# Kernel optimization log

Measured on AMD Instinct MI355X. Metric: run time of the kernel, lower is better.

Reference implementation:

```python
import jax, jax.numpy as jnp
import numpy as np

D_MODEL = 1024
NUM_HEADS = 16
PERIOD_LEN = 4096
HEAD_DIM = D_MODEL // NUM_HEADS


def setup_inputs() -> dict:
    key = jax.random.key(0)
    ks = jax.random.split(key, 10)
    B, S, D = 2, 2048, D_MODEL
    scale = 1.0 / np.sqrt(D)
    inp = {
        "x": jax.random.normal(ks[0], (B, S, D), dtype=jnp.float32),
        "wq": jax.random.normal(ks[1], (D, D), dtype=jnp.float32) * scale,
        "bq": jnp.zeros((D,), dtype=jnp.float32),
        "wk": jax.random.normal(ks[2], (D, D), dtype=jnp.float32) * scale,
        "bk": jnp.zeros((D,), dtype=jnp.float32),
        "wv": jax.random.normal(ks[3], (D, D), dtype=jnp.float32) * scale,
        "bv": jnp.zeros((D,), dtype=jnp.float32),
        "wo": jax.random.normal(ks[4], (D, D), dtype=jnp.float32) * scale,
        "bo": jnp.zeros((D,), dtype=jnp.float32),
        # original init is zeros; use small randn so bias path is non-trivial
        "rel_bias": jax.random.normal(ks[5], (PERIOD_LEN, NUM_HEADS), dtype=jnp.float32) * 0.02,
    }
    return inp


def reference(x, wq, bq, wk, bk, wv, bv, wo, bo, rel_bias):
    B, S, D = x.shape
    H, Hd = NUM_HEADS, HEAD_DIM
    q = (x @ wq + bq).reshape(B, S, H, Hd).transpose(0, 2, 1, 3)  # [B,H,S,Hd]
    k = (x @ wk + bk).reshape(B, S, H, Hd).transpose(0, 2, 1, 3)
    v = (x @ wv + bv).reshape(B, S, H, Hd).transpose(0, 2, 1, 3)
    scores = jnp.einsum('bhqd,bhkd->bhqk', q, k) / jnp.sqrt(jnp.float32(Hd))
    if S <= PERIOD_LEN:
        pos = jnp.arange(S)
        circ = (pos[:, None] - pos[None, :]) % PERIOD_LEN  # [S,S]
        bias = rel_bias[circ]                               # [S,S,H]
        scores = scores + bias.transpose(2, 0, 1)[None]     # [1,H,S,S]
    attn = jax.nn.softmax(scores, axis=-1)
    out = jnp.einsum('bhqk,bhkd->bhqd', attn, v)
    out = out.transpose(0, 2, 1, 3).reshape(B, S, D)
    return out @ wo + bo
```

## Files before the change

kernel.cpp:

```cpp
#include <hip/hip_runtime.h>
#include <hip/hip_bf16.h>

#define D_MODEL 1024
#define NHEADS  16
#define HEADD   64
#define SEQ     2048
#define PERIOD  4096
#define LOG2E   1.44269504088896340736f

typedef __attribute__((ext_vector_type(4)))  float f32x4;
typedef __attribute__((ext_vector_type(16))) float f32x16;
typedef __attribute__((ext_vector_type(4)))  float fvec4;
typedef __attribute__((ext_vector_type(8)))  short s16x8;
typedef __attribute__((ext_vector_type(4)))  short s16x4;
typedef __attribute__((ext_vector_type(2)))  int   i32x2;
typedef __attribute__((ext_vector_type(4)))  int   i32x4;

__device__ __forceinline__ short bf16_bits(float f) {
    union { float f; unsigned u; } v; v.f = f;
    unsigned r = v.u + 0x7FFFu + ((v.u >> 16) & 1u);
    return (short)(r >> 16);
}

__device__ __forceinline__ int cvt_pk_bf16(float a, float b) {
    int r;
    asm("v_cvt_pk_bf16_f32 %0, %1, %2" : "=v"(r) : "v"(a), "v"(b));
    return r;
}

__device__ __forceinline__ float exp2_hw(float x) {
    float r;
    asm("v_exp_f32 %0, %1" : "=v"(r) : "v"(x));
    return r;
}

__device__ __forceinline__ void gload_lds16(const void* g, void* l) {
    __builtin_amdgcn_global_load_lds(
        (const __attribute__((address_space(1))) void*)g,
        (__attribute__((address_space(3))) void*)l, 16, 0, 0);
}

__global__ void cvt_x(const float* __restrict__ x, short* __restrict__ xb) {
    int i = blockIdx.x * blockDim.x + threadIdx.x;
    fvec4 v = ((const fvec4*)x)[i];
    s16x4 o;
    o.x = bf16_bits(v.x); o.y = bf16_bits(v.y);
    o.z = bf16_bits(v.z); o.w = bf16_bits(v.w);
    ((s16x4*)xb)[i] = o;
}

__global__ void transpose_w4(const float* __restrict__ wq, const float* __restrict__ wk,
                             const float* __restrict__ wv, const float* __restrict__ wo,
                             short* __restrict__ wqkv, short* __restrict__ wot) {
    __shared__ float tile[64][65];
    int wsel = blockIdx.y;
    const float* src = wsel == 0 ? wq : (wsel == 1 ? wk : (wsel == 2 ? wv : wo));
    short* dst = wsel < 3 ? wqkv + wsel * 1024 * 1024 : wot;
    int bx = blockIdx.x & 15, by = blockIdx.x >> 4;
    int n0 = bx * 64, k0 = by * 64;
    int t = threadIdx.x;
    int cr = t >> 4;
    int cc = (t & 15) * 4;
    for (int i = 0; i < 4; ++i) {
        int row = cr + i * 16;
        fvec4 v = *(const fvec4*)&src[(k0 + row) * D_MODEL + n0 + cc];
        tile[row][cc+0] = v.x; tile[row][cc+1] = v.y;
        tile[row][cc+2] = v.z; tile[row][cc+3] = v.w;
    }
    __syncthreads();
    for (int i = 0; i < 4; ++i) {
        int row = cr + i * 16;
        s16x4 o;
        o.x = bf16_bits(tile[cc+0][row]);
        o.y = bf16_bits(tile[cc+1][row]);
        o.z = bf16_bits(tile[cc+2][row]);
        o.w = bf16_bits(tile[cc+3][row]);
        *(s16x4*)&dst[(n0 + row) * D_MODEL + k0 + cc] = o;
    }
}

__global__ void transpose_v(const short* __restrict__ vb, short* __restrict__ vt) {
    __shared__ short tile[64][80];
    int bh = blockIdx.y, st = blockIdx.x;
    int b = bh >> 4, h = bh & 15;
    int s0 = st * 64;
    int t = threadIdx.x;
    int row = t >> 3, ch = t & 7;
    for (int i = 0; i < 2; ++i) {
        int r = row + i * 32;
        *(s16x8*)&tile[r][ch * 8] =
            *(const s16x8*)&vb[(b * SEQ + s0 + r) * D_MODEL + h * HEADD + ch * 8];
    }
    __syncthreads();
    for (int i = 0; i < 2; ++i) {
        int d = row + i * 32;
        s16x8 o;
        #pragma unroll
        for (int j = 0; j < 8; ++j) o[j] = tile[ch * 8 + j][d];
        *(s16x8*)&vt[(b * D_MODEL + h * HEADD + d) * SEQ + s0 + ch * 8] = o;
    }
}

__global__ void build_biasq(const float* __restrict__ rb, f32x4* __restrict__ bq4) {
    int id = blockIdx.x * 256 + threadIdx.x;
    int h = id >> 12, a = id & 4095;
    f32x4 v;
    #pragma unroll
    for (int j = 0; j < 4; ++j)
        v[j] = rb[((a + j) & (PERIOD - 1)) * NHEADS + h] * LOG2E - 16.0f;
    bq4[id] = v;
}

__global__ __launch_bounds__(256, 3) void gemm_qkv(
    const short* __restrict__ A, const short* __restrict__ Bt,
    const float* __restrict__ biasq, const float* __restrict__ biask,
    const float* __restrict__ biasv,
    short* __restrict__ qb, short* __restrict__ kb, short* __restrict__ vb)
{
    __shared__ short As[2][128 * 64];
    __shared__ short Bs[2][64 * 64];
    int tid = threadIdx.x;
    int lane = tid & 63, wid = tid >> 6;
    int ln = lane & 15, g = lane >> 4;
    int wr = (wid >> 1) * 64, wc = (wid & 1) * 32;

    int bid = blockIdx.x;
    int xcd = bid & 7, slot = bid >> 3;
    int mb = xcd * 4 + (slot / 48);
    int nb = slot % 48;
    int m0 = mb * 128, n0 = nb * 64;

    int wsel = n0 >> 10;
    const float* bias = wsel == 0 ? biasq : (wsel == 1 ? biask : biasv);
    short* dst = wsel == 0 ? qb : (wsel == 1 ? kb : vb);
    float osc = wsel == 0 ? (0.125f * LOG2E) : 1.0f;
    int ncol0 = n0 & 1023;

    f32x4 acc[4][2] = {};

    auto STAGE = [&](int kt, int bi) {
        #pragma unroll
        for (int i = 0; i < 4; ++i) {
            int idx = i * 256 + tid;
            int row = idx >> 3, ch = idx & 7;
            int gch = ch ^ (row & 7);
            gload_lds16(&A[(m0 + row) * 1024 + kt + gch * 8],
                        (char*)&As[bi][0] + (i * 256 + wid * 64) * 16);
        }
        #pragma unroll
        for (int i = 0; i < 2; ++i) {
            int idx = i * 256 + tid;
            int row = idx >> 3, ch = idx & 7;
            int gch = ch ^ (row & 7);
            gload_lds16(&Bt[(n0 + row) * 1024 + kt + gch * 8],
                        (char*)&Bs[bi][0] + (i * 256 + wid * 64) * 16);
        }
    };

    STAGE(0, 0);
    __syncthreads();

    for (int kt = 0; kt < 16; ++kt) {
        int bi = kt & 1;
        if (kt < 15) STAGE((kt + 1) * 64, bi ^ 1);

        s16x8 af[4][2], bfr[2][2];
        #pragma unroll
        for (int m = 0; m < 4; ++m) {
            int row = wr + m * 16 + ln;
            #pragma unroll
            for (int kc = 0; kc < 2; ++kc)
                af[m][kc] = *(const s16x8*)&As[bi][row * 64 + (((kc * 4 + g) ^ (row & 7)) * 8)];
        }
        #pragma unroll
        for (int n = 0; n < 2; ++n) {
            int row = wc + n * 16 + ln;
            #pragma unroll
            for (int kc = 0; kc < 2; ++kc)
                bfr[n][kc] = *(const s16x8*)&Bs[bi][row * 64 + (((kc * 4 + g) ^ (row & 7)) * 8)];
        }
        #pragma unroll
        for (int kc = 0; kc < 2; ++kc)
            #pragma unroll
            for (int m = 0; m < 4; ++m)
                #pragma unroll
                for (int n = 0; n < 2; ++n)
                    acc[m][n] = __builtin_amdgcn_mfma_f32_16x16x32_bf16(af[m][kc], bfr[n][kc], acc[m][n], 0, 0, 0);

        __syncthreads();
    }

    #pragma unroll
    for (int m = 0; m < 4; ++m) {
        int gr0 = m0 + wr + m * 16 + g * 4;
        #pragma unroll
        for (int n = 0; n < 2; ++n) {
            int gc = ncol0 + wc + n * 16 + ln;
            float bvv = bias[gc];
            #pragma unroll
            for (int r = 0; r < 4; ++r)
                dst[(gr0 + r) * 1024 + gc] = bf16_bits((acc[m][n][r] + bvv) * osc);
        }
    }
}

template<int MODE>
__global__ __launch_bounds__(256) void gemm_bias(
    const short* __restrict__ A, const short* __restrict__ Bt,
    const float* __restrict__ bias, void* __restrict__ Cout)
{
    __shared__ short As[2][128 * 64];
    __shared__ short Bs[2][64 * 64];
    int tid = threadIdx.x;
    int lane = tid & 63, wid = tid >> 6;
    int ln = lane & 15, g = lane >> 4;
    int wr = (wid >> 1) * 64, wc = (wid & 1) * 32;

    int bid = blockIdx.x;
    int xcd = bid & 7, slot = bid >> 3;
    int mb = xcd * 4 + (slot >> 4);
    int nb = slot & 15;
    int m0 = mb * 128, n0 = nb * 64;

    f32x4 acc[4][2] = {};

    auto STAGE = [&](int kt, int bi) {
        #pragma unroll
        for (int i = 0; i < 4; ++i) {
            int idx = i * 256 + tid;
            int row = idx >> 3, ch = idx & 7;
            int gch = ch ^ (row & 7);
            gload_lds16(&A[(m0 + row) * 1024 + kt + gch * 8],
                        (char*)&As[bi][0] + (i * 256 + wid * 64) * 16);
        }
        #pragma unroll
        for (int i = 0; i < 2; ++i) {
            int idx = i * 256 + tid;
            int row = idx >> 3, ch = idx & 7;
            int gch = ch ^ (row & 7);
            gload_lds16(&Bt[(n0 + row) * 1024 + kt + gch * 8],
                        (char*)&Bs[bi][0] + (i * 256 + wid * 64) * 16);
        }
    };

    STAGE(0, 0);
    __syncthreads();

    for (int kt = 0; kt < 16; ++kt) {
        int bi = kt & 1;
        if (kt < 15) STAGE((kt + 1) * 64, bi ^ 1);

        s16x8 af[4][2], bfr[2][2];
        #pragma unroll
        for (int m = 0; m < 4; ++m) {
            int row = wr + m * 16 + ln;
            #pragma unroll
            for (int kc = 0; kc < 2; ++kc)
                af[m][kc] = *(const s16x8*)&As[bi][row * 64 + (((kc * 4 + g) ^ (row & 7)) * 8)];
        }
        #pragma unroll
        for (int n = 0; n < 2; ++n) {
            int row = wc + n * 16 + ln;
            #pragma unroll
            for (int kc = 0; kc < 2; ++kc)
                bfr[n][kc] = *(const s16x8*)&Bs[bi][row * 64 + (((kc * 4 + g) ^ (row & 7)) * 8)];
        }
        #pragma unroll
        for (int kc = 0; kc < 2; ++kc)
            #pragma unroll
            for (int m = 0; m < 4; ++m)
                #pragma unroll
                for (int n = 0; n < 2; ++n)
                    acc[m][n] = __builtin_amdgcn_mfma_f32_16x16x32_bf16(af[m][kc], bfr[n][kc], acc[m][n], 0, 0, 0);

        __syncthreads();
    }

    #pragma unroll
    for (int m = 0; m < 4; ++m) {
        int gr0 = m0 + wr + m * 16 + g * 4;
        #pragma unroll
        for (int n = 0; n < 2; ++n) {
            int gc = n0 + wc + n * 16 + ln;
            float bv = bias[gc];
            #pragma unroll
            for (int r = 0; r < 4; ++r) {
                int gr = gr0 + r;
                float v = acc[m][n][r] + bv;
                if (MODE == 0)      ((short*)Cout)[gr * 1024 + gc] = bf16_bits(v * (0.125f * LOG2E));
                else if (MODE == 1) ((short*)Cout)[gr * 1024 + gc] = bf16_bits(v);
                else                ((float*)Cout)[gr * 1024 + gc] = v;
            }
        }
    }
}

__global__ __launch_bounds__(256, 2) void attn_partial(
    const short* __restrict__ qb,
    const short* __restrict__ kb,
    const short* __restrict__ vt,
    const f32x4* __restrict__ biasq,
    float* __restrict__ po,
    float* __restrict__ pl)
{
    __shared__ short KV[2][2][64 * 64];

    int tid = threadIdx.x;
    int lane = tid & 63;
    int wid = tid >> 6;
    int l31 = lane & 31, hi = lane >> 5;

    int bid = blockIdx.x;
    int xcd = bid & 7, slot = bid >> 3;
    int hb = xcd * 4 + (slot >> 5);
    int qt = (slot >> 1) & 15;
    int half = slot & 1;
    int h = hb & 15, b = hb >> 4;
    int q0 = qt * 128 + wid * 32;
    int qrow = q0 + l31;
    int kbase = half * 1024;

    s16x8 aq[4];
    #pragma unroll
    for (int kk = 0; kk < 4; ++kk)
        aq[kk] = *(const s16x8*)&qb[(b * SEQ + qrow) * D_MODEL + h * HEADD + kk * 16 + hi * 8];

    const f32x4* bq = biasq + h * PERIOD;

    float lrow = 0.f;
    f32x16 ot[2] = {};

    auto STAGE = [&](int k0, int bi) {
        #pragma unroll
        for (int i = 0; i < 2; ++i) {
            int idx = i * 256 + tid;
            int row = idx >> 3, ch = idx & 7;
            int gch = ch ^ ((row & 7) ^ ((row >> 3) & 3));
            gload_lds16(&kb[(b * SEQ + k0 + row) * D_MODEL + h * HEADD + gch * 8],
                        (char*)&KV[bi][0][0] + (i * 256 + wid * 64) * 16);
            gload_lds16(&vt[(b * D_MODEL + h * HEADD + row) * SEQ + k0 + gch * 8],
                        (char*)&KV[bi][1][0] + (i * 256 + wid * 64) * 16);
        }
    };

    STAGE(kbase, 0);
    __syncthreads();

    for (int kt = 0; kt < 16; ++kt) {
        int k0 = kbase + kt * 64;
        int bi = kt & 1;
        if (kt < 15) STAGE(k0 + 64, bi ^ 1);

        f32x4 bv[2][4];
        #pragma unroll
        for (int kt32 = 0; kt32 < 2; ++kt32)
            #pragma unroll
            for (int rq = 0; rq < 4; ++rq) {
                int kq = k0 + kt32 * 32 + rq * 8 + hi * 4;
                bv[kt32][rq] = bq[(qrow - kq - 3) & (PERIOD - 1)];
            }

        f32x16 s[2];
        const short* Ksp = &KV[bi][0][0];
        const short* Vsp = &KV[bi][1][0];
        __builtin_amdgcn_s_setprio(1);
        #pragma unroll
        for (int kt32 = 0; kt32 < 2; ++kt32) {
            f32x16 acc = {};
            int rowK = kt32 * 32 + l31;
            int swz = (rowK & 7) ^ ((rowK >> 3) & 3);
            #pragma unroll
            for (int kk = 0; kk < 4; ++kk) {
                s16x8 kf = *(const s16x8*)&Ksp[rowK * 64 + (((2 * kk + hi) ^ swz) * 8)];
                acc = __builtin_amdgcn_mfma_f32_32x32x16_bf16(kf, aq[kk], acc, 0, 0, 0);
            }
            s[kt32] = acc;
        }
        __builtin_amdgcn_s_setprio(0);

        #pragma unroll
        for (int kt32 = 0; kt32 < 2; ++kt32)
            #pragma unroll
            for (int rq = 0; rq < 4; ++rq) {
                s[kt32][rq * 4 + 0] = exp2_hw(s[kt32][rq * 4 + 0] + bv[kt32][rq][3]);
                s[kt32][rq * 4 + 1] = exp2_hw(s[kt32][rq * 4 + 1] + bv[kt32][rq][2]);
                s[kt32][rq * 4 + 2] = exp2_hw(s[kt32][rq * 4 + 2] + bv[kt32][rq][1]);
                s[kt32][rq * 4 + 3] = exp2_hw(s[kt32][rq * 4 + 3] + bv[kt32][rq][0]);
            }

        float sm[16];
        #pragma unroll
        for (int t = 0; t < 16; ++t) sm[t] = s[0][t] + s[1][t];
        #pragma unroll
        for (int t = 0; t < 8; ++t) sm[t] += sm[t + 8];
        #pragma unroll
        for (int t = 0; t < 4; ++t) sm[t] += sm[t + 4];
        float psum = (sm[0] + sm[1]) + (sm[2] + sm[3]);
        {
            i32x2 r = __builtin_amdgcn_permlane32_swap(__float_as_int(psum), __float_as_int(psum), false, false);
            psum = __int_as_float(r[0]) + __int_as_float(r[1]);
        }
        lrow += psum;

        #pragma unroll
        for (int kt32 = 0; kt32 < 2; ++kt32) {
            int pk[8];
            #pragma unroll
            for (int i = 0; i < 8; ++i)
                pk[i] = cvt_pk_bf16(s[kt32][2 * i], s[kt32][2 * i + 1]);
            #pragma unroll
            for (int ks = 0; ks < 2; ++ks) {
                int a0 = pk[ks * 4 + 0], b0 = pk[ks * 4 + 2];
                int a1 = pk[ks * 4 + 1], b1 = pk[ks * 4 + 3];
                int a0s = __shfl_xor(a0, 32), b0s = __shfl_xor(b0, 32);
                int a1s = __shfl_xor(a1, 32), b1s = __shfl_xor(b1, 32);
                i32x4 wi;
                wi[0] = (lane < 32) ? a0 : b0s;
                wi[1] = (lane < 32) ? a1 : b1s;
                wi[2] = (lane < 32) ? a0s : b0;
                wi[3] = (lane < 32) ? a1s : b1;
                s16x8 pb = __builtin_bit_cast(s16x8, wi);
                __builtin_amdgcn_s_setprio(1);
                #pragma unroll
                for (int dd = 0; dd < 2; ++dd) {
                    int rowV = dd * 32 + l31;
                    int swzV = (rowV & 7) ^ ((rowV >> 3) & 3);
                    int chV = kt32 * 4 + ks * 2 + hi;
                    s16x8 vf = *(const s16x8*)&Vsp[rowV * 64 + ((chV ^ swzV) * 8)];
                    ot[dd] = __builtin_amdgcn_mfma_f32_32x32x16_bf16(vf, pb, ot[dd], 0, 0, 0);
                }
                __builtin_amdgcn_s_setprio(0);
            }
        }

        __syncthreads();
    }

    float* poH = po + half * (4096 * 1024);
    int obase = (b * SEQ + qrow) * D_MODEL + h * HEADD;
    #pragma unroll
    for (int dd = 0; dd < 2; ++dd)
        #pragma unroll
        for (int rq = 0; rq < 4; ++rq) {
            f32x4 st;
            st[0] = ot[dd][rq * 4 + 0];
            st[1] = ot[dd][rq * 4 + 1];
            st[2] = ot[dd][rq * 4 + 2];
            st[3] = ot[dd][rq * 4 + 3];
            *(f32x4*)&poH[obase + dd * 32 + rq * 8 + hi * 4] = st;
        }
    if (hi == 0)
        pl[half * (4096 * 16) + (b * SEQ + qrow) * 16 + h] = lrow;
}

__global__ __launch_bounds__(256) void attn_merge(
    const float* __restrict__ po, const float* __restrict__ pl,
    short* __restrict__ ao)
{
    int idx = blockIdx.x * 256 + threadIdx.x;
    int base = idx * 8;
    int row = base >> 10, col = base & 1023, h = col >> 6;
    float l = pl[row * 16 + h] + pl[4096 * 16 + row * 16 + h];
    float inv = 1.0f / l;
    const float* p0 = po + row * 1024 + col;
    const float* p1 = p0 + 4096 * 1024;
    f32x4 a0 = *(const f32x4*)p0;
    f32x4 a1 = *(const f32x4*)(p0 + 4);
    f32x4 b0 = *(const f32x4*)p1;
    f32x4 b1 = *(const f32x4*)(p1 + 4);
    i32x4 o;
    o[0] = cvt_pk_bf16((a0[0] + b0[0]) * inv, (a0[1] + b0[1]) * inv);
    o[1] = cvt_pk_bf16((a0[2] + b0[2]) * inv, (a0[3] + b0[3]) * inv);
    o[2] = cvt_pk_bf16((a1[0] + b1[0]) * inv, (a1[1] + b1[1]) * inv);
    o[3] = cvt_pk_bf16((a1[2] + b1[2]) * inv, (a1[3] + b1[3]) * inv);
    *(i32x4*)&ao[base] = o;
}

extern "C" void kernel_launch(void* const* d_in, const int* in_sizes, int n_in,
                              void* d_out, int out_size, void* d_ws, size_t ws_size,
                              hipStream_t stream) {
    const float* x  = (const float*)d_in[0];
    const float* wq = (const float*)d_in[1];
    const float* bq = (const float*)d_in[2];
    const float* wk = (const float*)d_in[3];
    const float* bk = (const float*)d_in[4];
    const float* wv = (const float*)d_in[5];
    const float* bv = (const float*)d_in[6];
    const float* wo = (const float*)d_in[7];
    const float* bo = (const float*)d_in[8];
    const float* rb = (const float*)d_in[9];

    char* ws = (char*)d_ws;
    short* xb   = (short*)(ws);
    short* wqkv = (short*)(ws + (8u  << 20));
    short* wot  = (short*)(ws + (14u << 20));
    short* qb   = (short*)(ws + (16u << 20));
    short* kb   = (short*)(ws + (24u << 20));
    short* vb   = (short*)(ws + (32u << 20));
    short* vt   = (short*)(ws + (40u << 20));
    f32x4* bqt  = (f32x4*)(ws + (32u << 20));
    float* po   = (float*)(ws + (48u << 20));
    float* pl   = (float*)(ws + (80u << 20));
    short* ao   = xb;

    cvt_x<<<4096, 256, 0, stream>>>(x, xb);
    transpose_w4<<<dim3(256, 4), 256, 0, stream>>>(wq, wk, wv, wo, wqkv, wot);

    gemm_qkv<<<1536, 256, 0, stream>>>(xb, wqkv, bq, bk, bv, qb, kb, vb);
    transpose_v<<<dim3(32, 32), 256, 0, stream>>>(vb, vt);
    build_biasq<<<256, 256, 0, stream>>>(rb, bqt);

    attn_partial<<<1024, 256, 0, stream>>>(qb, kb, vt, bqt, po, pl);
    attn_merge<<<2048, 256, 0, stream>>>(po, pl, ao);

    gemm_bias<3><<<512, 256, 0, stream>>>(ao, wot, bo, (float*)d_out);
}
```

Measured before the change: 140.8 us.

## Fuse attention partial merge into output projection GEMM A-tile staging

Removes the separate attn_merge kernel. The output GEMM now reads both fp32 partial-output halves and their row sums directly, normalizes them, converts to bf16 and writes the A tile into LDS. This saves one launch plus the write and re-read of the bf16 intermediate. The cost is that each fp32 partial tile is now re-read by every column block, which is several times more A-side traffic than the bf16 path, and the A load goes through registers instead of direct-to-LDS loads.

```diff
diff --git a/kernel.cpp b/kernel.cpp
--- a/kernel.cpp
+++ b/kernel.cpp
@@ -204,10 +204,11 @@
     }
 }
 
-template<int MODE>
-__global__ __launch_bounds__(256) void gemm_bias(
-    const short* __restrict__ A, const short* __restrict__ Bt,
-    const float* __restrict__ bias, void* __restrict__ Cout)
+__global__ __launch_bounds__(256) void gemm_out_merge(
+    const float* __restrict__ po,
+    const float* __restrict__ pl,
+    const short* __restrict__ Bt,
+    const float* __restrict__ bias, float* __restrict__ Cout)
 {
     __shared__ short As[2][128 * 64];
     __shared__ short Bs[2][64 * 64];
@@ -224,31 +225,58 @@
 
     f32x4 acc[4][2] = {};
 
-    auto STAGE = [&](int kt, int bi) {
+    auto STAGE_B = [&](int kt, int bi) {
+        #pragma unroll
+        for (int i = 0; i < 2; ++i) {
+            int idx = i * 256 + tid;
+            int row = idx >> 3, ch = idx & 7;
+            int gch = ch ^ (row & 7);
+            gload_lds16(&Bt[(n0 + row) * 1024 + kt * 64 + gch * 8],
+                        (char*)&Bs[bi][0] + (i * 256 + wid * 64) * 16);
+        }
+    };
+
+    f32x4 av0[4], av1[4], av2[4], av3[4];
+    float lv0[4], lv1[4];
+
+    auto ALOAD = [&](int kt) {
         #pragma unroll
         for (int i = 0; i < 4; ++i) {
             int idx = i * 256 + tid;
             int row = idx >> 3, ch = idx & 7;
             int gch = ch ^ (row & 7);
-            gload_lds16(&A[(m0 + row) * 1024 + kt + gch * 8],
-                        (char*)&As[bi][0] + (i * 256 + wid * 64) * 16);
-        }
-        #pragma unroll
-        for (int i = 0; i < 2; ++i) {
+            const float* p0 = &po[(m0 + row) * 1024 + kt * 64 + gch * 8];
+            av0[i] = *(const f32x4*)p0;
+            av1[i] = *(const f32x4*)(p0 + 4);
+            av2[i] = *(const f32x4*)(p0 + 4096 * 1024);
+            av3[i] = *(const f32x4*)(p0 + 4096 * 1024 + 4);
+            lv0[i] = pl[(m0 + row) * 16 + kt];
+            lv1[i] = pl[4096 * 16 + (m0 + row) * 16 + kt];
+        }
+    };
+
+    auto AWRITE = [&](int bi) {
+        #pragma unroll
+        for (int i = 0; i < 4; ++i) {
             int idx = i * 256 + tid;
-            int row = idx >> 3, ch = idx & 7;
-            int gch = ch ^ (row & 7);
-            gload_lds16(&Bt[(n0 + row) * 1024 + kt + gch * 8],
-                        (char*)&Bs[bi][0] + (i * 256 + wid * 64) * 16);
+            float inv = __builtin_amdgcn_rcpf(lv0[i] + lv1[i]);
+            i32x4 w;
+            w[0] = cvt_pk_bf16((av0[i][0] + av2[i][0]) * inv, (av0[i][1] + av2[i][1]) * inv);
+            w[1] = cvt_pk_bf16((av0[i][2] + av2[i][2]) * inv, (av0[i][3] + av2[i][3]) * inv);
+            w[2] = cvt_pk_bf16((av1[i][0] + av3[i][0]) * inv, (av1[i][1] + av3[i][1]) * inv);
+            w[3] = cvt_pk_bf16((av1[i][2] + av3[i][2]) * inv, (av1[i][3] + av3[i][3]) * inv);
+            *(i32x4*)((char*)&As[bi][0] + idx * 16) = w;
         }
     };
 
-    STAGE(0, 0);
+    STAGE_B(0, 0);
+    ALOAD(0);
+    AWRITE(0);
     __syncthreads();
 
     for (int kt = 0; kt < 16; ++kt) {
         int bi = kt & 1;
-        if (kt < 15) STAGE((kt + 1) * 64, bi ^ 1);
+        if (kt < 15) { STAGE_B(kt + 1, bi ^ 1); ALOAD(kt + 1); }
 
         s16x8 af[4][2], bfr[2][2];
         #pragma unroll
@@ -273,6 +301,7 @@
                 for (int n = 0; n < 2; ++n)
                     acc[m][n] = __builtin_amdgcn_mfma_f32_16x16x32_bf16(af[m][kc], bfr[n][kc], acc[m][n], 0, 0, 0);
 
+        if (kt < 15) AWRITE(bi ^ 1);
         __syncthreads();
     }
 
@@ -284,13 +313,8 @@
             int gc = n0 + wc + n * 16 + ln;
             float bv = bias[gc];
             #pragma unroll
-            for (int r = 0; r < 4; ++r) {
-                int gr = gr0 + r;
-                float v = acc[m][n][r] + bv;
-                if (MODE == 0)      ((short*)Cout)[gr * 1024 + gc] = bf16_bits(v * (0.125f * LOG2E));
-                else if (MODE == 1) ((short*)Cout)[gr * 1024 + gc] = bf16_bits(v);
-                else                ((float*)Cout)[gr * 1024 + gc] = v;
-            }
+            for (int r = 0; r < 4; ++r)
+                Cout[(gr0 + r) * 1024 + gc] = acc[m][n][r] + bv;
         }
     }
 }
@@ -453,29 +477,6 @@
         pl[half * (4096 * 16) + (b * SEQ + qrow) * 16 + h] = lrow;
 }
 
-__global__ __launch_bounds__(256) void attn_merge(
-    const float* __restrict__ po, const float* __restrict__ pl,
-    short* __restrict__ ao)
-{
-    int idx = blockIdx.x * 256 + threadIdx.x;
-    int base = idx * 8;
-    int row = base >> 10, col = base & 1023, h = col >> 6;
-    float l = pl[row * 16 + h] + pl[4096 * 16 + row * 16 + h];
-    float inv = 1.0f / l;
-    const float* p0 = po + row * 1024 + col;
-    const float* p1 = p0 + 4096 * 1024;
-    f32x4 a0 = *(const f32x4*)p0;
-    f32x4 a1 = *(const f32x4*)(p0 + 4);
-    f32x4 b0 = *(const f32x4*)p1;
-    f32x4 b1 = *(const f32x4*)(p1 + 4);
-    i32x4 o;
-    o[0] = cvt_pk_bf16((a0[0] + b0[0]) * inv, (a0[1] + b0[1]) * inv);
-    o[1] = cvt_pk_bf16((a0[2] + b0[2]) * inv, (a0[3] + b0[3]) * inv);
-    o[2] = cvt_pk_bf16((a1[0] + b1[0]) * inv, (a1[1] + b1[1]) * inv);
-    o[3] = cvt_pk_bf16((a1[2] + b1[2]) * inv, (a1[3] + b1[3]) * inv);
-    *(i32x4*)&ao[base] = o;
-}
-
 extern "C" void kernel_launch(void* const* d_in, const int* in_sizes, int n_in,
                               void* d_out, int out_size, void* d_ws, size_t ws_size,
                               hipStream_t stream) {
@@ -501,7 +502,6 @@
     f32x4* bqt  = (f32x4*)(ws + (32u << 20));
     float* po   = (float*)(ws + (48u << 20));
     float* pl   = (float*)(ws + (80u << 20));
-    short* ao   = xb;
 
     cvt_x<<<4096, 256, 0, stream>>>(x, xb);
     transpose_w4<<<dim3(256, 4), 256, 0, stream>>>(wq, wk, wv, wo, wqkv, wot);
@@ -511,7 +511,6 @@
     build_biasq<<<256, 256, 0, stream>>>(rb, bqt);
 
     attn_partial<<<1024, 256, 0, stream>>>(qb, kb, vt, bqt, po, pl);
-    attn_merge<<<2048, 256, 0, stream>>>(po, pl, ao);
-
-    gemm_bias<3><<<512, 256, 0, stream>>>(ao, wot, bo, (float*)d_out);
-}
+
+    gemm_out_merge<<<512, 256, 0, stream>>>(po, pl, wot, bo, (float*)d_out);
+}
```

Result: slower. 154.5 us (+9.7%).
